# Optimization experiments

Hardware: AMD Instinct MI355X
Metric: run time of the kernel (lower is better)

## Reference

```python
import jax, jax.numpy as jnp
import numpy as np

D_MODEL = 2048
N_HEADS = 16
HEAD_DIM = D_MODEL // N_HEADS  # 128
ROPE_THETA = 10000.0
BATCH = 2
SEQ_LEN = 2048  # == window_size -> dense causal SDPA path


def setup_inputs() -> dict:
    key = jax.random.key(0)
    ks = jax.random.split(key, 5)
    scale = 1.0 / np.sqrt(D_MODEL)
    x = jax.random.normal(ks[0], (BATCH, SEQ_LEN, D_MODEL), dtype=jnp.float32)
    # torch nn.Linear weights are stored (out_features, in_features); y = x @ W.T
    Wq = jax.random.normal(ks[1], (D_MODEL, D_MODEL), dtype=jnp.float32) * scale
    Wk = jax.random.normal(ks[2], (D_MODEL, D_MODEL), dtype=jnp.float32) * scale
    Wv = jax.random.normal(ks[3], (D_MODEL, D_MODEL), dtype=jnp.float32) * scale
    Wo = jax.random.normal(ks[4], (D_MODEL, D_MODEL), dtype=jnp.float32) * scale
    return {"x": x, "Wq": Wq, "Wk": Wk, "Wv": Wv, "Wo": Wo}


def _apply_rope(x):
    # x: [B, H, S, HEAD_DIM]; interleaved-pair RoPE, positions 0..S-1
    S = x.shape[2]
    inv_freq = 1.0 / (ROPE_THETA ** (jnp.arange(0, HEAD_DIM, 2, dtype=jnp.float32) / HEAD_DIM))
    t = jnp.arange(S, dtype=jnp.float32)
    freqs = jnp.outer(t, inv_freq)            # [S, HEAD_DIM//2]
    cos = jnp.cos(freqs)
    sin = jnp.sin(freqs)
    x1 = x[..., 0::2]
    x2 = x[..., 1::2]
    rot = jnp.stack([x1 * cos - x2 * sin, x1 * sin + x2 * cos], axis=-1)  # [B,H,S,hd/2,2]
    return rot.reshape(x.shape)


def reference(x, Wq, Wk, Wv, Wo):
    B, S, _ = x.shape
    q = (x @ Wq.T).reshape(B, S, N_HEADS, HEAD_DIM).transpose(0, 2, 1, 3)  # [B,H,S,D]
    k = (x @ Wk.T).reshape(B, S, N_HEADS, HEAD_DIM).transpose(0, 2, 1, 3)
    v = (x @ Wv.T).reshape(B, S, N_HEADS, HEAD_DIM).transpose(0, 2, 1, 3)
    q = _apply_rope(q)
    k = _apply_rope(k)
    scores = jnp.einsum("bhqd,bhkd->bhqk", q, k) / np.sqrt(HEAD_DIM).astype(np.float32)
    causal = jnp.tril(jnp.ones((S, S), dtype=bool))
    scores = jnp.where(causal, scores, -jnp.inf)
    attn = jax.nn.softmax(scores, axis=-1)
    out = jnp.einsum("bhqk,bhkd->bhqd", attn, v)
    out = out.transpose(0, 2, 1, 3).reshape(B, S, N_HEADS * HEAD_DIM)
    return out @ Wo.T
```

## Files before the change

### kernel.cpp

```cpp
#include <hip/hip_runtime.h>
#include <stdint.h>

#define D_MODEL 2048
#define SEQ     2048
#define BATCH   2
#define NHEAD   16
#define HD      128
#define MROWS   (BATCH*SEQ)

typedef short short8 __attribute__((ext_vector_type(8)));
typedef float f32x4  __attribute__((ext_vector_type(4)));

__device__ __forceinline__ unsigned short f2b(float f) {
  unsigned int u = __float_as_uint(f);
  u += 0x7fffu + ((u >> 16) & 1u);
  return (unsigned short)(u >> 16);
}
__device__ __forceinline__ float b2f(unsigned short s) {
  return __uint_as_float(((unsigned int)s) << 16);
}
__device__ __forceinline__ void gll16(const void* g, void* l) {
  __builtin_amdgcn_global_load_lds((const __attribute__((address_space(1))) void*)g,
                                   (__attribute__((address_space(3))) void*)l, 16, 0, 0);
}
__device__ __forceinline__ void barrier_nodrain() {
  asm volatile("" ::: "memory");
  __builtin_amdgcn_s_barrier();
  asm volatile("" ::: "memory");
}

__global__ __launch_bounds__(256) void cast_all(
    const float* __restrict__ x,  const float* __restrict__ Wq,
    const float* __restrict__ Wk, const float* __restrict__ Wv,
    const float* __restrict__ Wo, unsigned short* __restrict__ dst)
{
  size_t e = ((size_t)blockIdx.x * 256 + threadIdx.x) * 4;
  const size_t XN = (size_t)MROWS * D_MODEL;
  const size_t WN = (size_t)D_MODEL * D_MODEL;
  const float* src; size_t off;
  if (e < XN) { src = x; off = e; }
  else {
    size_t e2 = e - XN;
    int w = (int)(e2 >> 22);
    off = e2 & (WN - 1);
    src = (w == 0) ? Wq : (w == 1) ? Wk : (w == 2) ? Wv : Wo;
  }
  float4 v = *(const float4*)(src + off);
  ushort4 o;
  o.x = f2b(v.x); o.y = f2b(v.y); o.z = f2b(v.z); o.w = f2b(v.w);
  *(ushort4*)(dst + e) = o;
}

template<int BM, int BN>
__device__ __forceinline__ void gemm_pipe(
    const unsigned short* __restrict__ A, const unsigned short* __restrict__ Bw,
    unsigned short* __restrict__ As, unsigned short* __restrict__ Bs,
    int m0, int n0, int tid, f32x4 (&acc)[BM / 32][4])
{
  constexpr int K  = D_MODEL;
  constexpr int NT = K / 64;
  constexpr int LA = BM / 64, LB = BN / 64;
  constexpr int LT = LA + LB;
  constexpr int MI = BM / 32, MH = MI / 2;
  const int wave = tid >> 6, lane = tid & 63, l15 = lane & 15, quad = lane >> 4;
  const int wr = wave >> 2, wc = wave & 3;
  const int sw = l15 & 7;
  const int arow = wr * (BM / 2) + l15;
  const int brow = wc * (BN / 4) + l15;

  auto stage = [&](int buf, int t) {
    const int kt = t * 64;
    #pragma unroll
    for (int i = 0; i < LA; ++i) {
      int slot = i * 512 + tid;
      int row = slot >> 3, ch = slot & 7;
      gll16(A + (size_t)(m0 + row) * K + kt + ((ch ^ (row & 7)) * 8),
            As + (size_t)buf * (BM * 64) + (size_t)(i * 512 + wave * 64) * 8);
    }
    #pragma unroll
    for (int i = 0; i < LB; ++i) {
      int slot = i * 512 + tid;
      int row = slot >> 3, ch = slot & 7;
      gll16(Bw + (size_t)(n0 + row) * K + kt + ((ch ^ (row & 7)) * 8),
            Bs + (size_t)buf * (BN * 64) + (size_t)(i * 512 + wave * 64) * 8);
    }
  };

  stage(0, 0);
  stage(1, 1);

  short8 ah[MH][2], bf[4][2];

  #pragma unroll 1
  for (int t = 0; t < NT; ++t) {
    const int cur = t & 1;
    if (t < NT - 1) {
      if constexpr (LT == 8) asm volatile("s_waitcnt vmcnt(8)" ::: "memory");
      else                   asm volatile("s_waitcnt vmcnt(6)" ::: "memory");
    } else {
      asm volatile("s_waitcnt vmcnt(0)" ::: "memory");
    }
    barrier_nodrain();

    const unsigned short* as = As + cur * (BM * 64);
    const unsigned short* bs = Bs + cur * (BN * 64);

    #pragma unroll
    for (int mi = 0; mi < MH; ++mi)
      #pragma unroll
      for (int ks = 0; ks < 2; ++ks)
        ah[mi][ks] = *(const short8*)(as + (arow + mi * 16) * 64 + (((ks * 4 + quad) ^ sw) * 8));
    #pragma unroll
    for (int ni = 0; ni < 2; ++ni)
      #pragma unroll
      for (int ks = 0; ks < 2; ++ks)
        bf[ni][ks] = *(const short8*)(bs + (brow + ni * 16) * 64 + (((ks * 4 + quad) ^ sw) * 8));
    __builtin_amdgcn_s_setprio(1);
    #pragma unroll
    for (int mi = 0; mi < MH; ++mi)
      #pragma unroll
      for (int ni = 0; ni < 2; ++ni)
        #pragma unroll
        for (int ks = 0; ks < 2; ++ks)
          acc[mi][ni] = __builtin_amdgcn_mfma_f32_16x16x32_bf16(ah[mi][ks], bf[ni][ks], acc[mi][ni], 0, 0, 0);
    __builtin_amdgcn_s_setprio(0);

    #pragma unroll
    for (int ni = 2; ni < 4; ++ni)
      #pragma unroll
      for (int ks = 0; ks < 2; ++ks)
        bf[ni][ks] = *(const short8*)(bs + (brow + ni * 16) * 64 + (((ks * 4 + quad) ^ sw) * 8));
    __builtin_amdgcn_s_setprio(1);
    #pragma unroll
    for (int mi = 0; mi < MH; ++mi)
      #pragma unroll
      for (int ni = 2; ni < 4; ++ni)
        #pragma unroll
        for (int ks = 0; ks < 2; ++ks)
          acc[mi][ni] = __builtin_amdgcn_mfma_f32_16x16x32_bf16(ah[mi][ks], bf[ni][ks], acc[mi][ni], 0, 0, 0);
    __builtin_amdgcn_s_setprio(0);

    #pragma unroll
    for (int mi = 0; mi < MH; ++mi)
      #pragma unroll
      for (int ks = 0; ks < 2; ++ks)
        ah[mi][ks] = *(const short8*)(as + (arow + (mi + MH) * 16) * 64 + (((ks * 4 + quad) ^ sw) * 8));
    __builtin_amdgcn_s_setprio(1);
    #pragma unroll
    for (int mi = 0; mi < MH; ++mi)
      #pragma unroll
      for (int ni = 2; ni < 4; ++ni)
        #pragma unroll
        for (int ks = 0; ks < 2; ++ks)
          acc[mi + MH][ni] = __builtin_amdgcn_mfma_f32_16x16x32_bf16(ah[mi][ks], bf[ni][ks], acc[mi + MH][ni], 0, 0, 0);
    #pragma unroll
    for (int mi = 0; mi < MH; ++mi)
      #pragma unroll
      for (int ni = 0; ni < 2; ++ni)
        #pragma unroll
        for (int ks = 0; ks < 2; ++ks)
          acc[mi + MH][ni] = __builtin_amdgcn_mfma_f32_16x16x32_bf16(ah[mi][ks], bf[ni][ks], acc[mi + MH][ni], 0, 0, 0);
    __builtin_amdgcn_s_setprio(0);

    barrier_nodrain();
    if (t + 2 < NT) stage(cur, t + 2);
  }
}

__global__ __launch_bounds__(512, 2) void gemm_qkv2(
    const unsigned short* __restrict__ Axb, const unsigned short* __restrict__ Wqkv,
    unsigned short* __restrict__ Qh, unsigned short* __restrict__ Kh,
    unsigned short* __restrict__ Vt)
{
  __shared__ unsigned short As[2 * 256 * 64];
  __shared__ unsigned short Bs[2 * 256 * 64];
  const int m0 = blockIdx.y * 256, n0g = blockIdx.x * 256;
  f32x4 acc[8][4];
  #pragma unroll
  for (int i = 0; i < 8; ++i)
    #pragma unroll
    for (int j = 0; j < 4; ++j) acc[i][j] = (f32x4){0.f, 0.f, 0.f, 0.f};

  gemm_pipe<256, 256>(Axb, Wqkv, As, Bs, m0, n0g, threadIdx.x, acc);

  const int tid = threadIdx.x, wave = tid >> 6, lane = tid & 63;
  const int l15 = lane & 15, quad = lane >> 4, wr = wave >> 2, wc = wave & 3;
  const int z = n0g >> 11;
  if (z < 2) {
    unsigned short* dst = z ? Kh : Qh;
    #pragma unroll
    for (int mi = 0; mi < 8; ++mi)
      #pragma unroll
      for (int ni = 0; ni < 4; ++ni) {
        int row0 = m0 + wr * 128 + mi * 16 + quad * 4;
        int col  = (n0g + wc * 64 + ni * 16 + l15) & (D_MODEL - 1);
        int h = col >> 7, d = col & (HD - 1);
        #pragma unroll
        for (int r = 0; r < 4; ++r) {
          int m = row0 + r; int bb = m >> 11; int s = m & (SEQ - 1);
          dst[((size_t)(bb * NHEAD + h) * SEQ + s) * HD + d] = f2b(acc[mi][ni][r]);
        }
      }
  } else {
    #pragma unroll
    for (int mi = 0; mi < 8; ++mi)
      #pragma unroll
      for (int ni = 0; ni < 4; ++ni) {
        int row0 = m0 + wr * 128 + mi * 16 + quad * 4;
        int col  = (n0g + wc * 64 + ni * 16 + l15) & (D_MODEL - 1);
        int h = col >> 7, d = col & (HD - 1);
        int bb = row0 >> 11; int s = row0 & (SEQ - 1);
        ushort4 pk;
        pk.x = f2b(acc[mi][ni][0]); pk.y = f2b(acc[mi][ni][1]);
        pk.z = f2b(acc[mi][ni][2]); pk.w = f2b(acc[mi][ni][3]);
        *(ushort4*)(Vt + ((size_t)(bb * NHEAD + h) * HD + d) * SEQ + s) = pk;
      }
  }
}

__global__ __launch_bounds__(512, 2) void gemm_out2(
    const unsigned short* __restrict__ A, const unsigned short* __restrict__ Wo,
    float* __restrict__ C)
{
  __shared__ unsigned short As[2 * 128 * 64];
  __shared__ unsigned short Bs[2 * 256 * 64];
  const int m0 = blockIdx.y * 128, n0 = blockIdx.x * 256;
  f32x4 acc[4][4];
  #pragma unroll
  for (int i = 0; i < 4; ++i)
    #pragma unroll
    for (int j = 0; j < 4; ++j) acc[i][j] = (f32x4){0.f, 0.f, 0.f, 0.f};

  gemm_pipe<128, 256>(A, Wo, As, Bs, m0, n0, threadIdx.x, acc);

  const int tid = threadIdx.x, wave = tid >> 6, lane = tid & 63;
  const int l15 = lane & 15, quad = lane >> 4, wr = wave >> 2, wc = wave & 3;
  #pragma unroll
  for (int mi = 0; mi < 4; ++mi)
    #pragma unroll
    for (int ni = 0; ni < 4; ++ni) {
      int row0 = m0 + wr * 64 + mi * 16 + quad * 4;
      int col  = n0 + wc * 64 + ni * 16 + l15;
      #pragma unroll
      for (int r = 0; r < 4; ++r)
        C[(size_t)(row0 + r) * D_MODEL + col] = acc[mi][ni][r];
    }
}

__global__ __launch_bounds__(256) void rope_k(unsigned short* __restrict__ Qh,
                                              unsigned short* __restrict__ Kh)
{
  unsigned short* P = blockIdx.y ? Kh : Qh;
  int rid = blockIdx.x * 4 + (threadIdx.x >> 6);
  int i = threadIdx.x & 63;
  int s = rid & (SEQ - 1);
  size_t base = (size_t)rid * HD + 2 * i;
  float inv = exp2f(-(float)i * (13.287712379549449f / 64.0f));
  float ang = (float)s * inv;
  float sn, cs; sincosf(ang, &sn, &cs);
  unsigned int pk = *(const unsigned int*)(P + base);
  float x1 = b2f((unsigned short)(pk & 0xffffu));
  float x2 = b2f((unsigned short)(pk >> 16));
  unsigned short o0 = f2b(x1 * cs - x2 * sn);
  unsigned short o1 = f2b(x1 * sn + x2 * cs);
  *(unsigned int*)(P + base) = (unsigned int)o0 | ((unsigned int)o1 << 16);
}

__global__ __launch_bounds__(256) void attn_k(
    const unsigned short* __restrict__ Qh, const unsigned short* __restrict__ Kh,
    const unsigned short* __restrict__ Vt, unsigned short* __restrict__ Aout)
{
  __shared__ unsigned short Ks[64 * 128];
  __shared__ unsigned short Vs[128 * 64];
  __shared__ unsigned short sPb[4][16 * 72];
  const int tid = threadIdx.x;
  const int wave = tid >> 6, lane = tid & 63, l15 = lane & 15, quad = lane >> 4;
  const int bh = blockIdx.y;
  const int b = bh >> 4, h = bh & 15;
  const unsigned short* Qb = Qh + (size_t)bh * SEQ * HD;
  const unsigned short* Kb = Kh + (size_t)bh * SEQ * HD;
  const unsigned short* Vb = Vt + (size_t)bh * HD * SEQ;
  unsigned short* pw = &sPb[wave][0];
  const float scl = 0.08838834764831845f * 1.4426950408889634f;

  #pragma unroll
  for (int half = 0; half < 2; ++half) {
    const int tile = half ? (31 - blockIdx.x) : blockIdx.x;
    const int q0b = tile * 64;
    const int q0w = q0b + wave * 16;
    const int q = q0w + l15;

    short8 qf[4];
    #pragma unroll
    for (int c = 0; c < 4; ++c)
      qf[c] = *(const short8*)(Qb + (size_t)(q0w + l15) * HD + c * 32 + quad * 8);

    f32x4 o[8];
    #pragma unroll
    for (int dj = 0; dj < 8; ++dj) o[dj] = (f32x4){0.f, 0.f, 0.f, 0.f};
    float ms = -1e30f, ls = 0.f;

    const int trips = tile + 1;
    for (int it = 0; it < trips; ++it) {
      const int k0 = it * 64;
      __syncthreads();
      #pragma unroll
      for (int c = 0; c < 4; ++c) {
        int slot = c * 256 + tid;
        int kr = slot >> 4, pch = slot & 15;
        gll16(Kb + (size_t)(k0 + kr) * HD + ((pch ^ (kr & 15)) * 8), Ks + slot * 8);
      }
      #pragma unroll
      for (int c = 0; c < 4; ++c) {
        int slot = c * 256 + tid;
        int vr = slot >> 3, pch = slot & 7;
        gll16(Vb + (size_t)vr * SEQ + k0 + ((pch ^ (vr & 7)) * 8), Vs + slot * 8);
      }
      __syncthreads();

      f32x4 st[4];
      #pragma unroll
      for (int ni = 0; ni < 4; ++ni) st[ni] = (f32x4){0.f, 0.f, 0.f, 0.f};
      #pragma unroll
      for (int ni = 0; ni < 4; ++ni) {
        const int rowb = (ni * 16 + l15) * 128;
        #pragma unroll
        for (int c = 0; c < 4; ++c) {
          short8 kf = *(const short8*)(Ks + rowb + (((c * 4 + quad) ^ l15) * 8));
          st[ni] = __builtin_amdgcn_mfma_f32_16x16x32_bf16(kf, qf[c], st[ni], 0, 0, 0);
        }
      }

      if (k0 + 63 > q0w) {
        #pragma unroll
        for (int ni = 0; ni < 4; ++ni)
          #pragma unroll
          for (int r = 0; r < 4; ++r) {
            int k = k0 + ni * 16 + quad * 4 + r;
            if (k > q) st[ni][r] = -1e30f;
          }
      }

      float lm = -1e30f;
      #pragma unroll
      for (int ni = 0; ni < 4; ++ni)
        #pragma unroll
        for (int r = 0; r < 4; ++r) lm = fmaxf(lm, st[ni][r]);
      lm = fmaxf(lm, __shfl_xor(lm, 16, 64));
      lm = fmaxf(lm, __shfl_xor(lm, 32, 64));
      float mn = fmaxf(ms, lm);
      float al = exp2f((ms - mn) * scl);
      ms = mn;
      float nm = mn * scl;
      float rs = 0.f;
      #pragma unroll
      for (int ni = 0; ni < 4; ++ni)
        #pragma unroll
        for (int r = 0; r < 4; ++r) {
          float p = exp2f(fmaf(st[ni][r], scl, -nm));
          st[ni][r] = p;
          rs += p;
        }
      rs += __shfl_xor(rs, 16, 64);
      rs += __shfl_xor(rs, 32, 64);
      ls = ls * al + rs;
      #pragma unroll
      for (int dj = 0; dj < 8; ++dj) o[dj] *= al;

      #pragma unroll
      for (int ni = 0; ni < 4; ++ni) {
        ushort4 pk;
        pk.x = f2b(st[ni][0]); pk.y = f2b(st[ni][1]);
        pk.z = f2b(st[ni][2]); pk.w = f2b(st[ni][3]);
        *(ushort4*)(pw + l15 * 72 + ni * 16 + quad * 4) = pk;
      }
      short8 pf0 = *(const short8*)(pw + l15 * 72 + quad * 8);
      short8 pf1 = *(const short8*)(pw + l15 * 72 + 32 + quad * 8);

      #pragma unroll
      for (int dj = 0; dj < 8; ++dj) {
        const int vrow = (dj * 16 + l15) * 64;
        short8 v0 = *(const short8*)(Vs + vrow + (((quad) ^ (l15 & 7)) * 8));
        short8 v1 = *(const short8*)(Vs + vrow + (((4 + quad) ^ (l15 & 7)) * 8));
        o[dj] = __builtin_amdgcn_mfma_f32_16x16x32_bf16(v0, pf0, o[dj], 0, 0, 0);
        o[dj] = __builtin_amdgcn_mfma_f32_16x16x32_bf16(v1, pf1, o[dj], 0, 0, 0);
      }
    }

    float rl = 1.0f / ls;
    #pragma unroll
    for (int dj = 0; dj < 8; ++dj) {
      ushort4 pk;
      pk.x = f2b(o[dj][0] * rl); pk.y = f2b(o[dj][1] * rl);
      pk.z = f2b(o[dj][2] * rl); pk.w = f2b(o[dj][3] * rl);
      *(ushort4*)(Aout + ((size_t)(b * SEQ + q)) * D_MODEL + h * HD + dj * 16 + quad * 4) = pk;
    }
  }
}

extern "C" void kernel_launch(void* const* d_in, const int* in_sizes, int n_in,
                              void* d_out, int out_size, void* d_ws, size_t ws_size,
                              hipStream_t stream)
{
  const float* x  = (const float*)d_in[0];
  const float* Wq = (const float*)d_in[1];
  const float* Wk = (const float*)d_in[2];
  const float* Wv = (const float*)d_in[3];
  const float* Wo = (const float*)d_in[4];
  float* out = (float*)d_out;

  unsigned short* xb  = (unsigned short*)d_ws;
  unsigned short* wqb = xb  + 8388608;
  unsigned short* wkb = wqb + 4194304;
  unsigned short* wvb = wkb + 4194304;
  unsigned short* wob = wvb + 4194304;
  unsigned short* qh  = wob + 4194304;
  unsigned short* kh  = qh  + 8388608;
  unsigned short* vt  = kh  + 8388608;
  unsigned short* ao  = vt  + 8388608;

  (void)wkb; (void)wvb;
  cast_all<<<24576, 256, 0, stream>>>(x, Wq, Wk, Wv, Wo, xb);
  gemm_qkv2<<<dim3(24, 16), 512, 0, stream>>>(xb, wqb, qh, kh, vt);
  rope_k<<<dim3(16384, 2), 256, 0, stream>>>(qh, kh);
  attn_k<<<dim3(16, 32), 256, 0, stream>>>(qh, kh, vt, ao);
  gemm_out2<<<dim3(8, 32), 512, 0, stream>>>(ao, wob, out);
}
```

Before: 418.1 us.

## Rewrite GEMM main loop as half-tile ping-pong pipeline with staggered loads

Replaces the two-buffer, whole-tile GEMM pipeline with an 8-phase schedule that splits the A and B tiles into halves. Each quarter of the MFMA work is interleaved with a global-to-LDS prefetch of the next half-tile, using explicit vmcnt waits and barriers. The wave-to-row and wave-to-column mapping changes to interleaved 16-row and 16-column strips, and the epilogues are updated to match. The goal is to hide load latency and smooth out LDS traffic in the QKV and output projections. The cost is more barriers per K step and fragile hand-counted waitcnt values.

After: 410.2 us. Within noise of the previous version (-1.9%).

```diff
diff --git a/kernel.cpp b/kernel.cpp
--- a/kernel.cpp
+++ b/kernel.cpp
@@ -27,6 +27,17 @@
   asm volatile("" ::: "memory");
   __builtin_amdgcn_s_barrier();
   asm volatile("" ::: "memory");
+}
+template<int N> __device__ __forceinline__ void vmwait() {
+  if constexpr (N == 0)      asm volatile("s_waitcnt vmcnt(0)" ::: "memory");
+  else if constexpr (N == 1) asm volatile("s_waitcnt vmcnt(1)" ::: "memory");
+  else if constexpr (N == 2) asm volatile("s_waitcnt vmcnt(2)" ::: "memory");
+  else if constexpr (N == 3) asm volatile("s_waitcnt vmcnt(3)" ::: "memory");
+  else if constexpr (N == 4) asm volatile("s_waitcnt vmcnt(4)" ::: "memory");
+  else if constexpr (N == 5) asm volatile("s_waitcnt vmcnt(5)" ::: "memory");
+  else if constexpr (N == 6) asm volatile("s_waitcnt vmcnt(6)" ::: "memory");
+  else if constexpr (N == 7) asm volatile("s_waitcnt vmcnt(7)" ::: "memory");
+  else                       asm volatile("s_waitcnt vmcnt(8)" ::: "memory");
 }
 
 __global__ __launch_bounds__(256) void cast_all(
@@ -51,129 +62,146 @@
   *(ushort4*)(dst + e) = o;
 }
 
-template<int BM, int BN>
-__device__ __forceinline__ void gemm_pipe(
+template<int BM, int LA>
+__device__ __forceinline__ void gemm_8ph(
     const unsigned short* __restrict__ A, const unsigned short* __restrict__ Bw,
     unsigned short* __restrict__ As, unsigned short* __restrict__ Bs,
     int m0, int n0, int tid, f32x4 (&acc)[BM / 32][4])
 {
-  constexpr int K  = D_MODEL;
-  constexpr int NT = K / 64;
-  constexpr int LA = BM / 64, LB = BN / 64;
-  constexpr int LT = LA + LB;
-  constexpr int MI = BM / 32, MH = MI / 2;
+  constexpr int K = D_MODEL, NT = K / 64;
+  constexpr int HA = BM / 2;
+  constexpr int MI = BM / 32, MIH = MI / 2;
+  constexpr int AHALF = HA * 64;
+  constexpr int BHALF = 128 * 64;
+  constexpr int P2N = 2 * (LA + 2);
+  constexpr int P4N = 2 * LA + 2;
   const int wave = tid >> 6, lane = tid & 63, l15 = lane & 15, quad = lane >> 4;
   const int wr = wave >> 2, wc = wave & 3;
-  const int sw = l15 & 7;
-  const int arow = wr * (BM / 2) + l15;
-  const int brow = wc * (BN / 4) + l15;
-
-  auto stage = [&](int buf, int t) {
-    const int kt = t * 64;
+  const int rA = wr * 16 + l15;
+  const int rB = wc * 16 + l15;
+  const int swk = l15 & 7;
+
+  auto stA = [&](int buf, int h, int t) {
     #pragma unroll
     for (int i = 0; i < LA; ++i) {
-      int slot = i * 512 + tid;
-      int row = slot >> 3, ch = slot & 7;
-      gll16(A + (size_t)(m0 + row) * K + kt + ((ch ^ (row & 7)) * 8),
-            As + (size_t)buf * (BM * 64) + (size_t)(i * 512 + wave * 64) * 8);
-    }
-    #pragma unroll
-    for (int i = 0; i < LB; ++i) {
-      int slot = i * 512 + tid;
-      int row = slot >> 3, ch = slot & 7;
-      gll16(Bw + (size_t)(n0 + row) * K + kt + ((ch ^ (row & 7)) * 8),
-            Bs + (size_t)buf * (BN * 64) + (size_t)(i * 512 + wave * 64) * 8);
+      int slot = i * 512 + tid, rw = slot >> 3, ch = slot & 7;
+      gll16(A + (size_t)(m0 + h * HA + rw) * K + t * 64 + ((ch ^ (rw & 7)) * 8),
+            As + (buf * 2 + h) * AHALF + (i * 512 + wave * 64) * 8);
     }
   };
-
-  stage(0, 0);
-  stage(1, 1);
-
-  short8 ah[MH][2], bf[4][2];
+  auto stB = [&](int buf, int h, int t) {
+    #pragma unroll
+    for (int i = 0; i < 2; ++i) {
+      int slot = i * 512 + tid, rw = slot >> 3, ch = slot & 7;
+      gll16(Bw + (size_t)(n0 + h * 128 + rw) * K + t * 64 + ((ch ^ (rw & 7)) * 8),
+            Bs + (buf * 2 + h) * BHALF + (i * 512 + wave * 64) * 8);
+    }
+  };
+  auto ldA = [&](int buf, int h, int ml, int ks) -> short8 {
+    int rw = ml * 32 + rA;
+    return *(const short8*)(As + (buf * 2 + h) * AHALF + rw * 64 + (((ks * 4 + quad) ^ swk) * 8));
+  };
+  auto ldB = [&](int buf, int h, int nl, int ks) -> short8 {
+    int rw = nl * 64 + rB;
+    return *(const short8*)(Bs + (buf * 2 + h) * BHALF + rw * 64 + (((ks * 4 + quad) ^ swk) * 8));
+  };
+
+  stA(0, 0, 0); stB(0, 0, 0); stA(0, 1, 0); stB(0, 1, 0);
+  stA(1, 0, 1); stB(1, 1, 1);
+  vmwait<LA + 2>();
+  barrier_nodrain();
+
+  short8 ah[MIH][2], b0[2][2], b1[2][2];
 
   #pragma unroll 1
   for (int t = 0; t < NT; ++t) {
-    const int cur = t & 1;
-    if (t < NT - 1) {
-      if constexpr (LT == 8) asm volatile("s_waitcnt vmcnt(8)" ::: "memory");
-      else                   asm volatile("s_waitcnt vmcnt(6)" ::: "memory");
-    } else {
-      asm volatile("s_waitcnt vmcnt(0)" ::: "memory");
-    }
-    barrier_nodrain();
-
-    const unsigned short* as = As + cur * (BM * 64);
-    const unsigned short* bs = Bs + cur * (BN * 64);
-
-    #pragma unroll
-    for (int mi = 0; mi < MH; ++mi)
-      #pragma unroll
-      for (int ks = 0; ks < 2; ++ks)
-        ah[mi][ks] = *(const short8*)(as + (arow + mi * 16) * 64 + (((ks * 4 + quad) ^ sw) * 8));
-    #pragma unroll
-    for (int ni = 0; ni < 2; ++ni)
-      #pragma unroll
-      for (int ks = 0; ks < 2; ++ks)
-        bf[ni][ks] = *(const short8*)(bs + (brow + ni * 16) * 64 + (((ks * 4 + quad) ^ sw) * 8));
+    const int buf = t & 1;
+
+    #pragma unroll
+    for (int ml = 0; ml < MIH; ++ml) {
+      ah[ml][0] = ldA(buf, 0, ml, 0); ah[ml][1] = ldA(buf, 0, ml, 1);
+    }
+    #pragma unroll
+    for (int nl = 0; nl < 2; ++nl) {
+      b0[nl][0] = ldB(buf, 0, nl, 0); b0[nl][1] = ldB(buf, 0, nl, 1);
+    }
+    if (t + 1 < NT) stB(buf ^ 1, 0, t + 1);
+    barrier_nodrain();
+    asm volatile("s_waitcnt lgkmcnt(0)" ::: "memory");
+    __builtin_amdgcn_sched_barrier(0);
     __builtin_amdgcn_s_setprio(1);
     #pragma unroll
-    for (int mi = 0; mi < MH; ++mi)
-      #pragma unroll
-      for (int ni = 0; ni < 2; ++ni)
+    for (int ml = 0; ml < MIH; ++ml)
+      #pragma unroll
+      for (int nl = 0; nl < 2; ++nl)
         #pragma unroll
         for (int ks = 0; ks < 2; ++ks)
-          acc[mi][ni] = __builtin_amdgcn_mfma_f32_16x16x32_bf16(ah[mi][ks], bf[ni][ks], acc[mi][ni], 0, 0, 0);
+          acc[ml][nl] = __builtin_amdgcn_mfma_f32_16x16x32_bf16(ah[ml][ks], b0[nl][ks], acc[ml][nl], 0, 0, 0);
     __builtin_amdgcn_s_setprio(0);
-
-    #pragma unroll
-    for (int ni = 2; ni < 4; ++ni)
-      #pragma unroll
-      for (int ks = 0; ks < 2; ++ks)
-        bf[ni][ks] = *(const short8*)(bs + (brow + ni * 16) * 64 + (((ks * 4 + quad) ^ sw) * 8));
+    barrier_nodrain();
+
+    #pragma unroll
+    for (int nl = 0; nl < 2; ++nl) {
+      b1[nl][0] = ldB(buf, 1, nl, 0); b1[nl][1] = ldB(buf, 1, nl, 1);
+    }
+    if (t + 1 < NT) stA(buf ^ 1, 1, t + 1);
+    if (t == NT - 1) vmwait<0>(); else vmwait<P2N>();
+    barrier_nodrain();
+    asm volatile("s_waitcnt lgkmcnt(0)" ::: "memory");
+    __builtin_amdgcn_sched_barrier(0);
     __builtin_amdgcn_s_setprio(1);
     #pragma unroll
-    for (int mi = 0; mi < MH; ++mi)
-      #pragma unroll
-      for (int ni = 2; ni < 4; ++ni)
+    for (int ml = 0; ml < MIH; ++ml)
+      #pragma unroll
+      for (int nl = 0; nl < 2; ++nl)
         #pragma unroll
         for (int ks = 0; ks < 2; ++ks)
-          acc[mi][ni] = __builtin_amdgcn_mfma_f32_16x16x32_bf16(ah[mi][ks], bf[ni][ks], acc[mi][ni], 0, 0, 0);
+          acc[ml][2 + nl] = __builtin_amdgcn_mfma_f32_16x16x32_bf16(ah[ml][ks], b1[nl][ks], acc[ml][2 + nl], 0, 0, 0);
     __builtin_amdgcn_s_setprio(0);
-
-    #pragma unroll
-    for (int mi = 0; mi < MH; ++mi)
-      #pragma unroll
-      for (int ks = 0; ks < 2; ++ks)
-        ah[mi][ks] = *(const short8*)(as + (arow + (mi + MH) * 16) * 64 + (((ks * 4 + quad) ^ sw) * 8));
+    barrier_nodrain();
+
+    #pragma unroll
+    for (int ml = 0; ml < MIH; ++ml) {
+      ah[ml][0] = ldA(buf, 1, ml, 0); ah[ml][1] = ldA(buf, 1, ml, 1);
+    }
+    if (t + 2 < NT) stA(buf, 0, t + 2);
+    barrier_nodrain();
+    asm volatile("s_waitcnt lgkmcnt(0)" ::: "memory");
+    __builtin_amdgcn_sched_barrier(0);
     __builtin_amdgcn_s_setprio(1);
     #pragma unroll
-    for (int mi = 0; mi < MH; ++mi)
-      #pragma unroll
-      for (int ni = 2; ni < 4; ++ni)
+    for (int ml = 0; ml < MIH; ++ml)
+      #pragma unroll
+      for (int nl = 0; nl < 2; ++nl)
         #pragma unroll
         for (int ks = 0; ks < 2; ++ks)
-          acc[mi + MH][ni] = __builtin_amdgcn_mfma_f32_16x16x32_bf16(ah[mi][ks], bf[ni][ks], acc[mi + MH][ni], 0, 0, 0);
-    #pragma unroll
-    for (int mi = 0; mi < MH; ++mi)
-      #pragma unroll
-      for (int ni = 0; ni < 2; ++ni)
+          acc[MIH + ml][2 + nl] = __builtin_amdgcn_mfma_f32_16x16x32_bf16(ah[ml][ks], b1[nl][ks], acc[MIH + ml][2 + nl], 0, 0, 0);
+    __builtin_amdgcn_s_setprio(0);
+    barrier_nodrain();
+
+    if (t + 2 < NT) stB(buf, 1, t + 2);
+    if (t < NT - 1) { if (t == NT - 2) vmwait<LA>(); else vmwait<P4N>(); }
+    barrier_nodrain();
+    __builtin_amdgcn_s_setprio(1);
+    #pragma unroll
+    for (int ml = 0; ml < MIH; ++ml)
+      #pragma unroll
+      for (int nl = 0; nl < 2; ++nl)
         #pragma unroll
         for (int ks = 0; ks < 2; ++ks)
-          acc[mi + MH][ni] = __builtin_amdgcn_mfma_f32_16x16x32_bf16(ah[mi][ks], bf[ni][ks], acc[mi + MH][ni], 0, 0, 0);
+          acc[MIH + ml][nl] = __builtin_amdgcn_mfma_f32_16x16x32_bf16(ah[ml][ks], b0[nl][ks], acc[MIH + ml][nl], 0, 0, 0);
     __builtin_amdgcn_s_setprio(0);
-
-    barrier_nodrain();
-    if (t + 2 < NT) stage(cur, t + 2);
+    barrier_nodrain();
   }
 }
 
-__global__ __launch_bounds__(512, 2) void gemm_qkv2(
+__global__ __launch_bounds__(512, 2) void gemm_qkv3(
     const unsigned short* __restrict__ Axb, const unsigned short* __restrict__ Wqkv,
     unsigned short* __restrict__ Qh, unsigned short* __restrict__ Kh,
     unsigned short* __restrict__ Vt)
 {
-  __shared__ unsigned short As[2 * 256 * 64];
-  __shared__ unsigned short Bs[2 * 256 * 64];
+  __shared__ unsigned short As[2 * 2 * 128 * 64];
+  __shared__ unsigned short Bs[2 * 2 * 128 * 64];
   const int m0 = blockIdx.y * 256, n0g = blockIdx.x * 256;
   f32x4 acc[8][4];
   #pragma unroll
@@ -181,7 +209,7 @@
     #pragma unroll
     for (int j = 0; j < 4; ++j) acc[i][j] = (f32x4){0.f, 0.f, 0.f, 0.f};
 
-  gemm_pipe<256, 256>(Axb, Wqkv, As, Bs, m0, n0g, threadIdx.x, acc);
+  gemm_8ph<256, 2>(Axb, Wqkv, As, Bs, m0, n0g, threadIdx.x, acc);
 
   const int tid = threadIdx.x, wave = tid >> 6, lane = tid & 63;
   const int l15 = lane & 15, quad = lane >> 4, wr = wave >> 2, wc = wave & 3;
@@ -192,8 +220,8 @@
     for (int mi = 0; mi < 8; ++mi)
       #pragma unroll
       for (int ni = 0; ni < 4; ++ni) {
-        int row0 = m0 + wr * 128 + mi * 16 + quad * 4;
-        int col  = (n0g + wc * 64 + ni * 16 + l15) & (D_MODEL - 1);
+        int row0 = m0 + mi * 32 + wr * 16 + quad * 4;
+        int col  = (n0g + ni * 64 + wc * 16 + l15) & (D_MODEL - 1);
         int h = col >> 7, d = col & (HD - 1);
         #pragma unroll
         for (int r = 0; r < 4; ++r) {
@@ -206,8 +234,8 @@
     for (int mi = 0; mi < 8; ++mi)
       #pragma unroll
       for (int ni = 0; ni < 4; ++ni) {
-        int row0 = m0 + wr * 128 + mi * 16 + quad * 4;
-        int col  = (n0g + wc * 64 + ni * 16 + l15) & (D_MODEL - 1);
+        int row0 = m0 + mi * 32 + wr * 16 + quad * 4;
+        int col  = (n0g + ni * 64 + wc * 16 + l15) & (D_MODEL - 1);
         int h = col >> 7, d = col & (HD - 1);
         int bb = row0 >> 11; int s = row0 & (SEQ - 1);
         ushort4 pk;
@@ -218,12 +246,12 @@
   }
 }
 
-__global__ __launch_bounds__(512, 2) void gemm_out2(
+__global__ __launch_bounds__(512, 2) void gemm_out3(
     const unsigned short* __restrict__ A, const unsigned short* __restrict__ Wo,
     float* __restrict__ C)
 {
-  __shared__ unsigned short As[2 * 128 * 64];
-  __shared__ unsigned short Bs[2 * 256 * 64];
+  __shared__ unsigned short As[2 * 2 * 64 * 64];
+  __shared__ unsigned short Bs[2 * 2 * 128 * 64];
   const int m0 = blockIdx.y * 128, n0 = blockIdx.x * 256;
   f32x4 acc[4][4];
   #pragma unroll
@@ -231,7 +259,7 @@
     #pragma unroll
     for (int j = 0; j < 4; ++j) acc[i][j] = (f32x4){0.f, 0.f, 0.f, 0.f};
 
-  gemm_pipe<128, 256>(A, Wo, As, Bs, m0, n0, threadIdx.x, acc);
+  gemm_8ph<128, 1>(A, Wo, As, Bs, m0, n0, threadIdx.x, acc);
 
   const int tid = threadIdx.x, wave = tid >> 6, lane = tid & 63;
   const int l15 = lane & 15, quad = lane >> 4, wr = wave >> 2, wc = wave & 3;
@@ -239,8 +267,8 @@
   for (int mi = 0; mi < 4; ++mi)
     #pragma unroll
     for (int ni = 0; ni < 4; ++ni) {
-      int row0 = m0 + wr * 64 + mi * 16 + quad * 4;
-      int col  = n0 + wc * 64 + ni * 16 + l15;
+      int row0 = m0 + mi * 32 + wr * 16 + quad * 4;
+      int col  = n0 + ni * 64 + wc * 16 + l15;
       #pragma unroll
       for (int r = 0; r < 4; ++r)
         C[(size_t)(row0 + r) * D_MODEL + col] = acc[mi][ni][r];
@@ -421,8 +449,8 @@
 
   (void)wkb; (void)wvb;
   cast_all<<<24576, 256, 0, stream>>>(x, Wq, Wk, Wv, Wo, xb);
-  gemm_qkv2<<<dim3(24, 16), 512, 0, stream>>>(xb, wqb, qh, kh, vt);
+  gemm_qkv3<<<dim3(24, 16), 512, 0, stream>>>(xb, wqb, qh, kh, vt);
   rope_k<<<dim3(16384, 2), 256, 0, stream>>>(qh, kh);
   attn_k<<<dim3(16, 32), 256, 0, stream>>>(qh, kh, vt, ao);
-  gemm_out2<<<dim3(8, 32), 512, 0, stream>>>(ao, wob, out);
-}
+  gemm_out3<<<dim3(8, 32), 512, 0, stream>>>(ao, wob, out);
+}
```
